# Performance work log

Measured on AMD Instinct MI355X. Metric: run time of the kernel, lower is better.

The kernel has to match this reference:

```python
import jax, jax.numpy as jnp
import numpy as np

N = 50000
E = 625000


def sage_conv(x, edge_index, Wl, bl, Wr):
    # PyG SAGEConv (aggr='mean', root_weight=True): lin_l(mean_aggr(x_j)) + lin_r(x_i)
    src, dst = edge_index[0], edge_index[1]
    n = x.shape[0]
    msum = jax.ops.segment_sum(x[src], dst, num_segments=n)  # [N, d]
    cnt = jax.ops.segment_sum(jnp.ones((edge_index.shape[1],), x.dtype), dst, num_segments=n)
    mean = msum / jnp.maximum(cnt, 1.0)[:, None]
    return mean @ Wl + bl + x @ Wr


def setup_inputs() -> dict:
    key = jax.random.key(0)
    ks = jax.random.split(key, 16)
    d, half, out_dim = 128, 64, 128
    s = lambda fan: 1.0 / np.sqrt(fan)
    inp = {
        'x': jax.random.normal(ks[0], (N, d), jnp.float32),
        'edge_index_in': jax.random.randint(ks[1], (2, E), 0, N, jnp.int32),
        'edge_index_out': jax.random.randint(ks[2], (2, E), 0, N, jnp.int32),
    }
    i = 3
    for layer, prev in [(0, d), (1, out_dim)]:
        for pre in ('in_', 'out_'):
            inp[f'{pre}Wl{layer}'] = jax.random.normal(ks[i], (prev, half), jnp.float32) * s(prev); i += 1
            inp[f'{pre}bl{layer}'] = jnp.zeros((half,), jnp.float32)
            inp[f'{pre}Wr{layer}'] = jax.random.normal(ks[i], (prev, half), jnp.float32) * s(prev); i += 1
        cin = prev + 2 * half
        inp[f'comb_W{layer}'] = jax.random.normal(ks[i], (cin, out_dim), jnp.float32) * s(cin); i += 1
        inp[f'comb_b{layer}'] = jnp.zeros((out_dim,), jnp.float32)
    inp['final_W'] = jax.random.normal(ks[i], (out_dim, 1), jnp.float32) * s(out_dim)
    inp['final_b'] = jnp.zeros((1,), jnp.float32)
    return inp


def reference(x, edge_index_in, edge_index_out,
              in_Wl0, in_bl0, in_Wr0, out_Wl0, out_bl0, out_Wr0, comb_W0, comb_b0,
              in_Wl1, in_bl1, in_Wr1, out_Wl1, out_bl1, out_Wr1, comb_W1, comb_b1,
              final_W, final_b):
    relu = jax.nn.relu
    layers = [
        (in_Wl0, in_bl0, in_Wr0, out_Wl0, out_bl0, out_Wr0, comb_W0, comb_b0),
        (in_Wl1, in_bl1, in_Wr1, out_Wl1, out_bl1, out_Wr1, comb_W1, comb_b1),
    ]
    for iWl, ibl, iWr, oWl, obl, oWr, cW, cb in layers:
        h_in = relu(sage_conv(x, edge_index_in, iWl, ibl, iWr))
        h_out = relu(sage_conv(x, edge_index_out, oWl, obl, oWr))
        x = relu(jnp.concatenate([x, h_in, h_out], axis=-1) @ cW + cb)
    out = x @ final_W + final_b  # [N, 1]
    return jnp.squeeze(out)  # target_dim == 1 -> squeeze
```

## Files before the change

kernel.cpp:

```cpp
#include <hip/hip_runtime.h>
#include <hip/hip_fp16.h>

#define N_NODES 50000
#define D 128
#define HALF 64
#define E_EDGES 625000
#define CAP 64
#define M_BLK 64
#define NODE64_GRID ((N_NODES + M_BLK - 1) / M_BLK)

#define NBINS 196
#define BIN_NODES 256
#define BINCAP 4096
#define GA 98
#define CHUNK ((E_EDGES + GA - 1) / GA)
#define PARTA_GRID (2 * GA)

typedef unsigned short ushortT;
typedef unsigned int uintT;
using f16     = _Float16;
using half8   = __attribute__((ext_vector_type(8))) _Float16;
using half4v  = __attribute__((ext_vector_type(4))) _Float16;
using floatx4 = __attribute__((ext_vector_type(4))) float;

__device__ __forceinline__ int rfl(int v) { return __builtin_amdgcn_readfirstlane(v); }
__device__ __forceinline__ floatx4 mfma16(half8 a, half8 b, floatx4 c) {
    return __builtin_amdgcn_mfma_f32_16x16x32_f16(a, b, c, 0, 0, 0);
}

__device__ __forceinline__ half8 ldsA(const f16 (*Xw)[D], int lane, int ks) {
    int r = lane & 15;
    int cc = ks * 4 + (lane >> 4);
    return *(const half8*)&Xw[r][((cc ^ (r & 7)) << 3)];
}

__device__ __forceinline__ void stage_f32(f16 (*Xw)[D], const float* __restrict__ X,
                                          int nodeBase, int lane) {
#pragma unroll
    for (int r4 = 0; r4 < 8; ++r4) {
        int s = lane + 64 * r4;
        int row = s >> 5, c4 = s & 31;
        int nn = nodeBase + row; if (nn > N_NODES - 1) nn = N_NODES - 1;
        float4 v = *(const float4*)(X + (size_t)nn * D + c4 * 4);
        int cc = c4 >> 1;
        half4v pk = { (f16)v.x, (f16)v.y, (f16)v.z, (f16)v.w };
        *(half4v*)&Xw[row][((cc ^ (row & 7)) << 3) + ((c4 & 1) << 2)] = pk;
    }
}

__device__ __forceinline__ void stage_f16(f16 (*Xw)[D], const f16* __restrict__ X,
                                          int nodeBase, int lane) {
#pragma unroll
    for (int r = 0; r < 4; ++r) {
        int s = lane + 64 * r;
        int row = s >> 4, cc = s & 15;
        int nn = nodeBase + row; if (nn > N_NODES - 1) nn = N_NODES - 1;
        uint4 v = *(const uint4*)(X + (size_t)nn * D + cc * 8);
        *(uint4*)&Xw[row][((cc ^ (row & 7)) << 3)] = v;
    }
}

__device__ __forceinline__ void gemm_store_P(const f16 (*Xw)[D], const f16* __restrict__ Wp,
                                             f16* __restrict__ Pout, int nodeBase, int lane) {
    half8 a[4];
#pragma unroll
    for (int ks = 0; ks < 4; ++ks) a[ks] = ldsA(Xw, lane, ks);
#pragma unroll
    for (int ct = 0; ct < 8; ++ct) {
        floatx4 acc = {0.f, 0.f, 0.f, 0.f};
#pragma unroll
        for (int ks = 0; ks < 4; ++ks) {
            half8 b = *(const half8*)(Wp + (((ct * 4 + ks) * 64 + lane) << 3));
            acc = mfma16(a[ks], b, acc);
        }
        int col = ct * 16 + (lane & 15);
#pragma unroll
        for (int i = 0; i < 4; ++i) {
            int nn = nodeBase + (lane >> 4) * 4 + i;
            if (nn < N_NODES) Pout[(size_t)nn * D + col] = (f16)acc[i];
        }
    }
}

__global__ __launch_bounds__(256) void prep_kernel(
    int* __restrict__ gcur,
    const float* iWr0, const float* oWr0, const float* iWl1, const float* oWl1,
    const float* iWr1, const float* oWr1, const float* iWl0, const float* oWl0,
    const float* cW0, const float* cW1,
    f16* Wr0p, f16* Wl1p, f16* Wr1p, f16* Wl0p, f16* cW0p, f16* cW1p)
{
    int b = blockIdx.x;
    if (b < 64) {
        for (int i = b * 256 + threadIdx.x; i < 2 * NBINS; i += 64 * 256) gcur[i] = 0;
        return;
    }
    b -= 64;
    if (b < 32) {
        int w = b >> 3;
        int e = (b & 7) * 256 + threadIdx.x;
        const float* Wa; const float* Wb; f16* dst;
        if (w == 0)      { Wa = iWr0; Wb = oWr0; dst = Wr0p; }
        else if (w == 1) { Wa = iWl1; Wb = oWl1; dst = Wl1p; }
        else if (w == 2) { Wa = iWr1; Wb = oWr1; dst = Wr1p; }
        else             { Wa = iWl0; Wb = oWl0; dst = Wl0p; }
        int lane = e & 63, ks = (e >> 6) & 3, ct = e >> 8;
        int k0 = ks * 32 + ((lane >> 4) << 3), c = ct * 16 + (lane & 15);
        half8 v;
#pragma unroll
        for (int j = 0; j < 8; ++j) {
            int k = k0 + j;
            float f = (c < 64) ? Wa[k * HALF + c] : Wb[k * HALF + (c - 64)];
            v[j] = (f16)f;
        }
        *(half8*)(dst + ((size_t)e << 3)) = v;
        return;
    }
    b -= 32;
    {
        int w = b >> 4;
        int e = (b & 15) * 256 + threadIdx.x;
        const float* W = w ? cW1 : cW0;
        f16* dst = w ? cW1p : cW0p;
        int lane = e & 63, ks = (e >> 6) & 7, ct = e >> 9;
        int k0 = ks * 32 + ((lane >> 4) << 3), c = ct * 16 + (lane & 15);
        half8 v;
#pragma unroll
        for (int j = 0; j < 8; ++j) v[j] = (f16)W[(size_t)(k0 + j) * D + c];
        *(half8*)(dst + ((size_t)e << 3)) = v;
    }
}

__global__ __launch_bounds__(256) void part_transform_kernel(
    const int* __restrict__ ei_in, const int* __restrict__ ei_out,
    int* __restrict__ gcur, uintT* __restrict__ part,
    const float* __restrict__ X, const f16* __restrict__ Wl0p, f16* __restrict__ P)
{
    __shared__ __align__(16) char lraw[28032];
    const int tid = threadIdx.x;
    if ((int)blockIdx.x < PARTA_GRID) {
        uintT* le   = (uintT*)lraw;
        int* cnt_l  = (int*)(lraw + 25600);
        int* base_l = cnt_l + NBINS;
        int* run_l  = base_l + NBINS;
        const int set = (int)blockIdx.x >= GA;
        const int b = blockIdx.x - (set ? GA : 0);
        const int* ei = set ? ei_out : ei_in;
        const int e0 = b * CHUNK;
        int n = E_EDGES - e0; if (n > CHUNK) n = CHUNK; if (n < 0) n = 0;
        for (int j = tid; j < n; j += 256) {
            int src = ei[e0 + j];
            int dst = ei[E_EDGES + e0 + j];
            le[j] = ((uintT)dst << 16) | (uintT)src;
        }
        for (int j = tid; j < NBINS; j += 256) cnt_l[j] = 0;
        __syncthreads();
        for (int j = tid; j < n; j += 256) atomicAdd(&cnt_l[le[j] >> 24], 1);
        __syncthreads();
        for (int j = tid; j < NBINS; j += 256) {
            int c = cnt_l[j];
            base_l[j] = c ? atomicAdd(&gcur[set * NBINS + j], c) : 0;
            run_l[j] = 0;
        }
        __syncthreads();
        uintT* pbase = part + (size_t)set * NBINS * BINCAP;
        for (int j = tid; j < n; j += 256) {
            uintT v = le[j];
            int bin = v >> 24;
            int pos = base_l[bin] + atomicAdd(&run_l[bin], 1);
            if (pos < BINCAP) pbase[(size_t)bin * BINCAP + pos] = v;
        }
        return;
    }
    f16 (*Xh)[16][D] = (f16(*)[16][D])lraw;
    const int bid = blockIdx.x - PARTA_GRID;
    const int wave = tid >> 6, lane = tid & 63;
    const int nodeBase = bid * M_BLK + wave * 16;
    f16 (*Xw)[D] = Xh[wave];
    stage_f32(Xw, X, nodeBase, lane);
    gemm_store_P(Xw, Wl0p, P, nodeBase, lane);
}

__global__ __launch_bounds__(256) void bucket_build_kernel(
    const uintT* __restrict__ part, const int* __restrict__ gcur,
    int* __restrict__ cnt_in, int* __restrict__ cnt_out,
    ushortT* __restrict__ bkt_in, ushortT* __restrict__ bkt_out)
{
    __shared__ ushortT bk[BIN_NODES * CAP];
    __shared__ int cl[BIN_NODES];
    const int tid = threadIdx.x;
    const int set = (int)blockIdx.x >= NBINS;
    const int bin = blockIdx.x - (set ? NBINS : 0);
    int total = gcur[set * NBINS + bin]; if (total > BINCAP) total = BINCAP;
    const uintT* pb = part + ((size_t)set * NBINS + bin) * BINCAP;
    cl[tid] = 0;
    __syncthreads();
    for (int j = tid; j < total; j += 256) {
        uintT v = pb[j];
        int loc = (v >> 16) & 255;
        int pos = atomicAdd(&cl[loc], 1);
        if (pos < CAP) bk[loc * CAP + pos] = (ushortT)(v & 0xFFFF);
    }
    __syncthreads();
    const int node0 = bin * BIN_NODES;
    int* cnt = set ? cnt_out : cnt_in;
    ushortT* bkt = set ? bkt_out : bkt_in;
    if (node0 + tid < N_NODES) cnt[node0 + tid] = cl[tid];
    const uint4* s4 = (const uint4*)bk;
    uint4* d4 = (uint4*)(bkt + (size_t)node0 * CAP);
    int lim = N_NODES - node0; if (lim > BIN_NODES) lim = BIN_NODES;
    lim = lim * (CAP / 8);
    for (int j = tid; j < lim; j += 256) d4[j] = s4[j];
}

__global__ __launch_bounds__(256) void pull_dual_kernel(
    const f16* __restrict__ P,
    const int* __restrict__ cnt_in, const ushortT* __restrict__ bkt_in,
    const int* __restrict__ cnt_out, const ushortT* __restrict__ bkt_out,
    f16* __restrict__ agg_in, f16* __restrict__ agg_out)
{
    int gid = blockIdx.x * blockDim.x + threadIdx.x;
    int wid = gid >> 6;
    const int lane = gid & 63;
    const int sub = lane >> 3;
    const int c = lane & 7;
    const int* cnt; const ushortT* bkt; f16* agg; int coloff;
    if (wid < N_NODES) { cnt = cnt_in; bkt = bkt_in; agg = agg_in; coloff = 0; }
    else { wid -= N_NODES; cnt = cnt_out; bkt = bkt_out; agg = agg_out; coloff = HALF; }
    const int node = rfl(wid);
    int deg = rfl(cnt[node]); if (deg > CAP) deg = CAP;
    const ushortT* row = bkt + (size_t)node * CAP;
    const f16* Pb = P + coloff + c * 8;
    float acc[8];
#pragma unroll
    for (int t = 0; t < 8; ++t) acc[t] = 0.0f;
    for (int j = 0; j < deg; j += 8) {
        int jc = j + sub;
        int idx = row[jc < deg ? jc : deg - 1];
        float m = (jc < deg) ? 1.0f : 0.0f;
        half8 v = *(const half8*)(Pb + (size_t)idx * D);
#pragma unroll
        for (int t = 0; t < 8; ++t) acc[t] = fmaf(m, (float)v[t], acc[t]);
    }
#pragma unroll
    for (int t = 0; t < 8; ++t) {
        acc[t] += __shfl_xor(acc[t], 8, 64);
        acc[t] += __shfl_xor(acc[t], 16, 64);
        acc[t] += __shfl_xor(acc[t], 32, 64);
    }
    if (sub == 0) {
        float inv = 1.0f / fmaxf((float)deg, 1.0f);
        half8 o;
#pragma unroll
        for (int t = 0; t < 8; ++t) o[t] = (f16)(acc[t] * inv);
        *(half8*)(agg + (size_t)node * HALF + c * 8) = o;
    }
}

__global__ __launch_bounds__(256) void fused_mfma_kernel(
    const float* __restrict__ Xf, const f16* __restrict__ X16,
    const f16* __restrict__ AGI, const f16* __restrict__ AGO,
    const f16* __restrict__ Wrp, const float* __restrict__ bl_in, const float* __restrict__ bl_out,
    const f16* __restrict__ cWp, const float* __restrict__ cb,
    f16* __restrict__ Xout16,
    const f16* __restrict__ Wlnp, f16* __restrict__ Pout,
    const float* __restrict__ fW, const float* __restrict__ fb, float* __restrict__ outv)
{
    __shared__ f16 Xh[4][16][D];
    __shared__ f16 Hh[4][16][D];
    const int tid = threadIdx.x, wave = tid >> 6, lane = tid & 63;
    const int nodeBase = blockIdx.x * M_BLK + wave * 16;
    f16 (*Xw)[D] = Xh[wave];
    f16 (*Hw)[D] = Hh[wave];
    const int colq = lane & 15;
    const int rq = lane >> 4;

    if (Xf) stage_f32(Xw, Xf, nodeBase, lane);
    else    stage_f16(Xw, X16, nodeBase, lane);

    half8 aX[4];
#pragma unroll
    for (int ks = 0; ks < 4; ++ks) aX[ks] = ldsA(Xw, lane, ks);

#pragma unroll
    for (int ct = 0; ct < 8; ++ct) {
        floatx4 acc = {0.f, 0.f, 0.f, 0.f};
#pragma unroll
        for (int ks = 0; ks < 4; ++ks) {
            half8 b = *(const half8*)(Wrp + (((ct * 4 + ks) * 64 + lane) << 3));
            acc = mfma16(aX[ks], b, acc);
        }
        int c64 = (ct & 3) * 16 + colq;
        const f16* AG = (ct < 4) ? AGI : AGO;
        float bl = (ct < 4) ? bl_in[c64] : bl_out[c64];
        int colg = ct * 16 + colq;
        int cc = colg >> 3;
#pragma unroll
        for (int i = 0; i < 4; ++i) {
            int r16 = rq * 4 + i;
            int nn = nodeBase + r16; if (nn > N_NODES - 1) nn = N_NODES - 1;
            float h = acc[i] + (float)AG[(size_t)nn * HALF + c64] + bl;
            Hw[r16][((cc ^ (r16 & 7)) << 3) + (colg & 7)] = (f16)fmaxf(h, 0.f);
        }
    }

    floatx4 acc2[8];
#pragma unroll
    for (int ct = 0; ct < 8; ++ct) {
        float cbv = cb[ct * 16 + colq];
        floatx4 t = {cbv, cbv, cbv, cbv};
#pragma unroll
        for (int ks = 0; ks < 4; ++ks) {
            half8 b = *(const half8*)(cWp + (((ct * 8 + ks) * 64 + lane) << 3));
            t = mfma16(aX[ks], b, t);
        }
        acc2[ct] = t;
    }
    half8 aH[4];
#pragma unroll
    for (int ks = 0; ks < 4; ++ks) aH[ks] = ldsA(Hw, lane, ks);
#pragma unroll
    for (int ct = 0; ct < 8; ++ct) {
#pragma unroll
        for (int ks = 0; ks < 4; ++ks) {
            half8 b = *(const half8*)(cWp + (((ct * 8 + 4 + ks) * 64 + lane) << 3));
            acc2[ct] = mfma16(aH[ks], b, acc2[ct]);
        }
    }

    if (fW == nullptr) {
#pragma unroll
        for (int ct = 0; ct < 8; ++ct) {
            int colg = ct * 16 + colq;
            int cc = colg >> 3;
#pragma unroll
            for (int i = 0; i < 4; ++i) {
                int r16 = rq * 4 + i;
                int nn = nodeBase + r16;
                f16 hv = (f16)fmaxf(acc2[ct][i], 0.f);
                if (nn < N_NODES) Xout16[(size_t)nn * D + colg] = hv;
                Xw[r16][((cc ^ (r16 & 7)) << 3) + (colg & 7)] = hv;
            }
        }
        gemm_store_P(Xw, Wlnp, Pout, nodeBase, lane);
    } else {
        float fs0 = 0, fs1 = 0, fs2 = 0, fs3 = 0;
#pragma unroll
        for (int ct = 0; ct < 8; ++ct) {
            float fwv = fW[ct * 16 + colq];
            fs0 = fmaf(fmaxf(acc2[ct][0], 0.f), fwv, fs0);
            fs1 = fmaf(fmaxf(acc2[ct][1], 0.f), fwv, fs1);
            fs2 = fmaf(fmaxf(acc2[ct][2], 0.f), fwv, fs2);
            fs3 = fmaf(fmaxf(acc2[ct][3], 0.f), fwv, fs3);
        }
#pragma unroll
        for (int off = 1; off < 16; off <<= 1) {
            fs0 += __shfl_xor(fs0, off, 64);
            fs1 += __shfl_xor(fs1, off, 64);
            fs2 += __shfl_xor(fs2, off, 64);
            fs3 += __shfl_xor(fs3, off, 64);
        }
        if (colq == 0) {
            float fbv = fb[0];
            int nb = nodeBase + rq * 4;
            if (nb + 0 < N_NODES) outv[nb + 0] = fs0 + fbv;
            if (nb + 1 < N_NODES) outv[nb + 1] = fs1 + fbv;
            if (nb + 2 < N_NODES) outv[nb + 2] = fs2 + fbv;
            if (nb + 3 < N_NODES) outv[nb + 3] = fs3 + fbv;
        }
    }
}

extern "C" void kernel_launch(void* const* d_in, const int* in_sizes, int n_in,
                              void* d_out, int out_size, void* d_ws, size_t ws_size,
                              hipStream_t stream) {
    const float* x       = (const float*)d_in[0];
    const int*   ei_in   = (const int*)d_in[1];
    const int*   ei_out  = (const int*)d_in[2];
    const float* in_Wl0  = (const float*)d_in[3];
    const float* in_bl0  = (const float*)d_in[4];
    const float* in_Wr0  = (const float*)d_in[5];
    const float* out_Wl0 = (const float*)d_in[6];
    const float* out_bl0 = (const float*)d_in[7];
    const float* out_Wr0 = (const float*)d_in[8];
    const float* comb_W0 = (const float*)d_in[9];
    const float* comb_b0 = (const float*)d_in[10];
    const float* in_Wl1  = (const float*)d_in[11];
    const float* in_bl1  = (const float*)d_in[12];
    const float* in_Wr1  = (const float*)d_in[13];
    const float* out_Wl1 = (const float*)d_in[14];
    const float* out_bl1 = (const float*)d_in[15];
    const float* out_Wr1 = (const float*)d_in[16];
    const float* comb_W1 = (const float*)d_in[17];
    const float* comb_b1 = (const float*)d_in[18];
    const float* final_W = (const float*)d_in[19];
    const float* final_b = (const float*)d_in[20];
    float* out = (float*)d_out;

    char* wsb = (char*)d_ws;
    size_t off = 0;
    auto take = [&](size_t sz) -> char* {
        char* p = wsb + off;
        off += (sz + 255) & ~(size_t)255;
        return p;
    };
    f16* AGI       = (f16*)take((size_t)N_NODES * HALF * 2);
    f16* AGO       = (f16*)take((size_t)N_NODES * HALF * 2);
    f16* X1h       = (f16*)take((size_t)N_NODES * D * 2);
    f16* P         = (f16*)take((size_t)N_NODES * D * 2);
    int* cnt_in    = (int*)take((size_t)2 * N_NODES * 4);
    int* cnt_out   = cnt_in + N_NODES;
    ushortT* bkt_in  = (ushortT*)take((size_t)N_NODES * CAP * 2);
    ushortT* bkt_out = (ushortT*)take((size_t)N_NODES * CAP * 2);
    int* gcur      = (int*)take((size_t)2 * NBINS * 4);
    uintT* part    = (uintT*)take((size_t)2 * NBINS * BINCAP * 4);
    f16* Wr0p = (f16*)take(32768);
    f16* Wl1p = (f16*)take(32768);
    f16* Wr1p = (f16*)take(32768);
    f16* Wl0p = (f16*)take(32768);
    f16* cW0p = (f16*)take(65536);
    f16* cW1p = (f16*)take(65536);

    const dim3 blk(256);
    const int pull_grid = (2 * N_NODES * 64) / 256;

    prep_kernel<<<128, blk, 0, stream>>>(
        gcur,
        in_Wr0, out_Wr0, in_Wl1, out_Wl1, in_Wr1, out_Wr1, in_Wl0, out_Wl0,
        comb_W0, comb_W1,
        Wr0p, Wl1p, Wr1p, Wl0p, cW0p, cW1p);

    part_transform_kernel<<<PARTA_GRID + NODE64_GRID, blk, 0, stream>>>(
        ei_in, ei_out, gcur, part, x, Wl0p, P);

    bucket_build_kernel<<<2 * NBINS, blk, 0, stream>>>(
        part, gcur, cnt_in, cnt_out, bkt_in, bkt_out);

    pull_dual_kernel<<<pull_grid, blk, 0, stream>>>(P, cnt_in, bkt_in, cnt_out, bkt_out, AGI, AGO);
    fused_mfma_kernel<<<NODE64_GRID, blk, 0, stream>>>(
        x, nullptr, AGI, AGO, Wr0p, in_bl0, out_bl0, cW0p, comb_b0,
        X1h, Wl1p, P, nullptr, nullptr, nullptr);

    pull_dual_kernel<<<pull_grid, blk, 0, stream>>>(P, cnt_in, bkt_in, cnt_out, bkt_out, AGI, AGO);
    fused_mfma_kernel<<<NODE64_GRID, blk, 0, stream>>>(
        nullptr, X1h, AGI, AGO, Wr1p, in_bl1, out_bl1, cW1p, comb_b1,
        nullptr, nullptr, nullptr, final_W, final_b, out);
}
```

Measured before the change: 182.0 us.

## Split fused MFMA kernel output columns across wave pairs per row group

```diff
diff --git a/kernel.cpp b/kernel.cpp
--- a/kernel.cpp
+++ b/kernel.cpp
@@ -8,6 +8,7 @@
 #define CAP 64
 #define M_BLK 64
 #define NODE64_GRID ((N_NODES + M_BLK - 1) / M_BLK)
+#define FUSED_GRID ((N_NODES + 31) / 32)
 
 #define NBINS 196
 #define BIN_NODES 256
@@ -48,12 +49,26 @@
     }
 }
 
-__device__ __forceinline__ void stage_f16(f16 (*Xw)[D], const f16* __restrict__ X,
-                                          int nodeBase, int lane) {
-#pragma unroll
-    for (int r = 0; r < 4; ++r) {
+__device__ __forceinline__ void stage_f32_half(f16 (*Xw)[D], const float* __restrict__ X,
+                                               int nodeBase, int lane, int t) {
+#pragma unroll
+    for (int r4 = 0; r4 < 4; ++r4) {
+        int s = lane + 64 * r4;
+        int row = t * 8 + (s >> 5), c4 = s & 31;
+        int nn = nodeBase + row; if (nn > N_NODES - 1) nn = N_NODES - 1;
+        float4 v = *(const float4*)(X + (size_t)nn * D + c4 * 4);
+        int cc = c4 >> 1;
+        half4v pk = { (f16)v.x, (f16)v.y, (f16)v.z, (f16)v.w };
+        *(half4v*)&Xw[row][((cc ^ (row & 7)) << 3) + ((c4 & 1) << 2)] = pk;
+    }
+}
+
+__device__ __forceinline__ void stage_f16_half(f16 (*Xw)[D], const f16* __restrict__ X,
+                                               int nodeBase, int lane, int t) {
+#pragma unroll
+    for (int r = 0; r < 2; ++r) {
         int s = lane + 64 * r;
-        int row = s >> 4, cc = s & 15;
+        int row = t * 8 + (s >> 4), cc = s & 15;
         int nn = nodeBase + row; if (nn > N_NODES - 1) nn = N_NODES - 1;
         uint4 v = *(const uint4*)(X + (size_t)nn * D + cc * 8);
         *(uint4*)&Xw[row][((cc ^ (row & 7)) << 3)] = v;
@@ -265,35 +280,40 @@
     const f16* __restrict__ Wlnp, f16* __restrict__ Pout,
     const float* __restrict__ fW, const float* __restrict__ fb, float* __restrict__ outv)
 {
-    __shared__ f16 Xh[4][16][D];
-    __shared__ f16 Hh[4][16][D];
+    __shared__ f16 Xh[2][16][D];
+    __shared__ f16 Hh[2][16][D];
+    __shared__ float fpart[2][2][16];
     const int tid = threadIdx.x, wave = tid >> 6, lane = tid & 63;
-    const int nodeBase = blockIdx.x * M_BLK + wave * 16;
-    f16 (*Xw)[D] = Xh[wave];
-    f16 (*Hw)[D] = Hh[wave];
+    const int rg = wave >> 1;
+    const int t  = wave & 1;
+    const int nodeBase = blockIdx.x * 32 + rg * 16;
+    f16 (*Xw)[D] = Xh[rg];
+    f16 (*Hw)[D] = Hh[rg];
     const int colq = lane & 15;
     const int rq = lane >> 4;
 
-    if (Xf) stage_f32(Xw, Xf, nodeBase, lane);
-    else    stage_f16(Xw, X16, nodeBase, lane);
+    if (Xf) stage_f32_half(Xw, Xf, nodeBase, lane, t);
+    else    stage_f16_half(Xw, X16, nodeBase, lane, t);
+    __syncthreads();
 
     half8 aX[4];
 #pragma unroll
     for (int ks = 0; ks < 4; ++ks) aX[ks] = ldsA(Xw, lane, ks);
 
 #pragma unroll
-    for (int ct = 0; ct < 8; ++ct) {
+    for (int ct4 = 0; ct4 < 4; ++ct4) {
+        const int ct = t * 4 + ct4;
         floatx4 acc = {0.f, 0.f, 0.f, 0.f};
 #pragma unroll
         for (int ks = 0; ks < 4; ++ks) {
             half8 b = *(const half8*)(Wrp + (((ct * 4 + ks) * 64 + lane) << 3));
             acc = mfma16(aX[ks], b, acc);
         }
-        int c64 = (ct & 3) * 16 + colq;
-        const f16* AG = (ct < 4) ? AGI : AGO;
-        float bl = (ct < 4) ? bl_in[c64] : bl_out[c64];
-        int colg = ct * 16 + colq;
-        int cc = colg >> 3;
+        const int c64 = ct4 * 16 + colq;
+        const f16* AG = t ? AGO : AGI;
+        const float bl = t ? bl_out[c64] : bl_in[c64];
+        const int colg = ct * 16 + colq;
+        const int cc = colg >> 3;
 #pragma unroll
         for (int i = 0; i < 4; ++i) {
             int r16 = rq * 4 + i;
@@ -303,54 +323,79 @@
         }
     }
 
-    floatx4 acc2[8];
-#pragma unroll
-    for (int ct = 0; ct < 8; ++ct) {
+    floatx4 acc2[4];
+#pragma unroll
+    for (int ct4 = 0; ct4 < 4; ++ct4) {
+        const int ct = t * 4 + ct4;
         float cbv = cb[ct * 16 + colq];
-        floatx4 t = {cbv, cbv, cbv, cbv};
+        floatx4 a = {cbv, cbv, cbv, cbv};
 #pragma unroll
         for (int ks = 0; ks < 4; ++ks) {
             half8 b = *(const half8*)(cWp + (((ct * 8 + ks) * 64 + lane) << 3));
-            t = mfma16(aX[ks], b, t);
-        }
-        acc2[ct] = t;
-    }
+            a = mfma16(aX[ks], b, a);
+        }
+        acc2[ct4] = a;
+    }
+    __syncthreads();
+
     half8 aH[4];
 #pragma unroll
     for (int ks = 0; ks < 4; ++ks) aH[ks] = ldsA(Hw, lane, ks);
 #pragma unroll
-    for (int ct = 0; ct < 8; ++ct) {
+    for (int ct4 = 0; ct4 < 4; ++ct4) {
+        const int ct = t * 4 + ct4;
 #pragma unroll
         for (int ks = 0; ks < 4; ++ks) {
             half8 b = *(const half8*)(cWp + (((ct * 8 + 4 + ks) * 64 + lane) << 3));
-            acc2[ct] = mfma16(aH[ks], b, acc2[ct]);
+            acc2[ct4] = mfma16(aH[ks], b, acc2[ct4]);
         }
     }
 
     if (fW == nullptr) {
 #pragma unroll
-        for (int ct = 0; ct < 8; ++ct) {
-            int colg = ct * 16 + colq;
-            int cc = colg >> 3;
+        for (int ct4 = 0; ct4 < 4; ++ct4) {
+            const int ct = t * 4 + ct4;
+            const int colg = ct * 16 + colq;
+            const int cc = colg >> 3;
 #pragma unroll
             for (int i = 0; i < 4; ++i) {
                 int r16 = rq * 4 + i;
                 int nn = nodeBase + r16;
-                f16 hv = (f16)fmaxf(acc2[ct][i], 0.f);
+                f16 hv = (f16)fmaxf(acc2[ct4][i], 0.f);
                 if (nn < N_NODES) Xout16[(size_t)nn * D + colg] = hv;
                 Xw[r16][((cc ^ (r16 & 7)) << 3) + (colg & 7)] = hv;
             }
         }
-        gemm_store_P(Xw, Wlnp, Pout, nodeBase, lane);
+        __syncthreads();
+        half8 a2[4];
+#pragma unroll
+        for (int ks = 0; ks < 4; ++ks) a2[ks] = ldsA(Xw, lane, ks);
+#pragma unroll
+        for (int ct4 = 0; ct4 < 4; ++ct4) {
+            const int ct = t * 4 + ct4;
+            floatx4 acc = {0.f, 0.f, 0.f, 0.f};
+#pragma unroll
+            for (int ks = 0; ks < 4; ++ks) {
+                half8 b = *(const half8*)(Wlnp + (((ct * 4 + ks) * 64 + lane) << 3));
+                acc = mfma16(a2[ks], b, acc);
+            }
+            const int col = ct * 16 + colq;
+#pragma unroll
+            for (int i = 0; i < 4; ++i) {
+                int nn = nodeBase + rq * 4 + i;
+                if (nn < N_NODES) Pout[(size_t)nn * D + col] = (f16)acc[i];
+            }
+        }
     } else {
         float fs0 = 0, fs1 = 0, fs2 = 0, fs3 = 0;
 #pragma unroll
-        for (int ct = 0; ct < 8; ++ct) {
+        for (int ct4 = 0; ct4 < 4; ++ct4) {
+            const int ct = t * 4 + ct4;
             float fwv = fW[ct * 16 + colq];
-            fs0 = fmaf(fmaxf(acc2[ct][0], 0.f), fwv, fs0);
-            fs1 = fmaf(fmaxf(acc2[ct][1], 0.f), fwv, fs1);
-            fs2 = fmaf(fmaxf(acc2[ct][2], 0.f), fwv, fs2);
-            fs3 = fmaf(fmaxf(acc2[ct][3], 0.f), fwv, fs3);
+            fs0 = fmaf(fmaxf(acc2[ct4][0], 0.f), fwv, fs0);
+            fs1 = fmaf(fmaxf(acc2[ct4][1], 0.f), fwv, fs1);
+            fs2 = fmaf(fmaxf(acc2[ct4][2], 0.f), fwv, fs2);
+            fs3 = fmaf(fmaxf(acc2[ct4][3], 0.f), fwv, fs3);
         }
 #pragma unroll
         for (int off = 1; off < 16; off <<= 1) {
@@ -360,12 +405,16 @@
             fs3 += __shfl_xor(fs3, off, 64);
         }
         if (colq == 0) {
-            float fbv = fb[0];
-            int nb = nodeBase + rq * 4;
-            if (nb + 0 < N_NODES) outv[nb + 0] = fs0 + fbv;
-            if (nb + 1 < N_NODES) outv[nb + 1] = fs1 + fbv;
-            if (nb + 2 < N_NODES) outv[nb + 2] = fs2 + fbv;
-            if (nb + 3 < N_NODES) outv[nb + 3] = fs3 + fbv;
+            fpart[rg][t][rq * 4 + 0] = fs0;
+            fpart[rg][t][rq * 4 + 1] = fs1;
+            fpart[rg][t][rq * 4 + 2] = fs2;
+            fpart[rg][t][rq * 4 + 3] = fs3;
+        }
+        __syncthreads();
+        if (t == 0 && lane < 16) {
+            int nn = nodeBase + lane;
+            if (nn < N_NODES)
+                outv[nn] = fpart[rg][0][lane] + fpart[rg][1][lane] + fb[0];
         }
     }
 }
@@ -436,12 +485,12 @@
         part, gcur, cnt_in, cnt_out, bkt_in, bkt_out);
 
     pull_dual_kernel<<<pull_grid, blk, 0, stream>>>(P, cnt_in, bkt_in, cnt_out, bkt_out, AGI, AGO);
-    fused_mfma_kernel<<<NODE64_GRID, blk, 0, stream>>>(
+    fused_mfma_kernel<<<FUSED_GRID, blk, 0, stream>>>(
         x, nullptr, AGI, AGO, Wr0p, in_bl0, out_bl0, cW0p, comb_b0,
         X1h, Wl1p, P, nullptr, nullptr, nullptr);
 
     pull_dual_kernel<<<pull_grid, blk, 0, stream>>>(P, cnt_in, bkt_in, cnt_out, bkt_out, AGI, AGO);
-    fused_mfma_kernel<<<NODE64_GRID, blk, 0, stream>>>(
+    fused_mfma_kernel<<<FUSED_GRID, blk, 0, stream>>>(
         nullptr, X1h, AGI, AGO, Wr1p, in_bl1, out_bl1, cW1p, comb_b1,
         nullptr, nullptr, nullptr, final_W, final_b, out);
 }
```

Result: faster. 151.7 us (median of 2 runs) (-16.7%).
